# Optimization experiments

Measured on AMD Instinct MI355X. Metric: run time of the kernel, lower is better.

## Reference

```python
import jax, jax.numpy as jnp
import numpy as np

EPS = 1e-6

def rms_norm(x, weight):
    # torch RMSNorm: norm in float32, cast back, then scale
    xf = x.astype(jnp.float32)
    normed = xf * jax.lax.rsqrt(jnp.mean(xf * xf, axis=-1, keepdims=True) + EPS)
    return normed.astype(x.dtype) * weight

def setup_inputs() -> dict:
    B, S, E = 2, 4096, 2048
    H, D, M = 16, 128, 1024  # n_heads, head_dim, memory slots; H*D == E
    key = jax.random.key(0)
    ks = jax.random.split(key, 8)
    std = 0.02
    return {
        "query_input": jax.random.normal(ks[0], (B, S, E), dtype=jnp.float32),
        "W_in": jax.random.normal(ks[1], (H * D, E), dtype=jnp.float32) * std,   # input_proj weight (out,in)
        "W_q": jax.random.normal(ks[2], (D, D), dtype=jnp.float32) * std,
        "W_k": jax.random.normal(ks[3], (D, D), dtype=jnp.float32) * std,
        "W_v": jax.random.normal(ks[4], (D, D), dtype=jnp.float32) * std,
        "stored_patterns": jax.random.normal(ks[5], (H, M, D), dtype=jnp.float32) * std,
        "norm_query_w": jnp.ones((E,), dtype=jnp.float32),
        "norm_retrieved_w": jnp.ones((H * D,), dtype=jnp.float32),
        "beta": jnp.asarray(1.0, dtype=jnp.float32),
    }

def reference(query_input, W_in, W_q, W_k, W_v, stored_patterns,
              norm_query_w, norm_retrieved_w, beta):
    B, S, E = query_input.shape
    H, M, D = stored_patterns.shape
    # RMSNorm + input projection
    normed_q = rms_norm(query_input, norm_query_w)
    proj = normed_q @ W_in.T                       # [B,S,H*D]
    q = proj.reshape(B, S, H, D) @ W_q.T           # [B,S,H,D]
    # memory-bank key/value projections (shared across batch)
    k = stored_patterns @ W_k.T                    # [H,M,D]
    v = stored_patterns @ W_v.T                    # [H,M,D]
    b = jax.nn.sigmoid(beta)                       # clamp_beta=True
    scores = jnp.einsum('bshd,hmd->bhsm', q * b, k)  # [B,H,S,M]
    probs = jax.nn.softmax(scores, axis=-1)
    attn_out = jnp.einsum('bhsm,hmd->bshd', probs, v)  # [B,S,H,D]
    attn_flat = attn_out.reshape(B, S, H * D)
    retrieved = rms_norm(attn_flat, norm_retrieved_w)
    # combine_method == 'add': residual add with original query input
    return retrieved + query_input
```

## Files before the change

### kernel.cpp

```cpp
#include <hip/hip_runtime.h>

typedef unsigned short u16;
typedef unsigned int u32;
typedef __attribute__((ext_vector_type(8))) short bf16x8;
typedef __attribute__((ext_vector_type(4))) float f32x4;
typedef __attribute__((ext_vector_type(16))) float f32x16;

#define B_ 2
#define S_ 4096
#define E_ 2048
#define H_ 16
#define D_ 128
#define M_ 1024
#define N_ROWS (B_*S_)

__device__ __forceinline__ u16 f2bf(float f) {
  unsigned u = __float_as_uint(f);
  u += 0x7FFF + ((u >> 16) & 1);
  return (u16)(u >> 16);
}
__device__ __forceinline__ float bf2f(u16 h) {
  return __uint_as_float(((unsigned)h) << 16);
}
__device__ __forceinline__ void gl_lds16(const u16* g, u16* l) {
  __builtin_amdgcn_global_load_lds(
      (const __attribute__((address_space(1))) u32*)g,
      (__attribute__((address_space(3))) u32*)l, 16, 0, 0);
}

__global__ __launch_bounds__(256) void rmsnorm_to_bf16(
    const float* __restrict__ x, const float* __restrict__ w, u16* __restrict__ out)
{
  int row = blockIdx.x;
  int t = threadIdx.x;
  const float* xr = x + (long)row * E_;
  float4 v0 = *(const float4*)(xr + t*8);
  float4 v1 = *(const float4*)(xr + t*8 + 4);
  float ss = v0.x*v0.x + v0.y*v0.y + v0.z*v0.z + v0.w*v0.w
           + v1.x*v1.x + v1.y*v1.y + v1.z*v1.z + v1.w*v1.w;
  for (int m = 1; m < 64; m <<= 1) ss += __shfl_xor(ss, m);
  __shared__ float red[4];
  if ((t & 63) == 0) red[t >> 6] = ss;
  __syncthreads();
  float tot = red[0] + red[1] + red[2] + red[3];
  float inv = rsqrtf(tot * (1.0f / E_) + 1e-6f);
  float4 w0 = *(const float4*)(w + t*8);
  float4 w1 = *(const float4*)(w + t*8 + 4);
  u16 o[8];
  o[0]=f2bf(v0.x*inv*w0.x); o[1]=f2bf(v0.y*inv*w0.y);
  o[2]=f2bf(v0.z*inv*w0.z); o[3]=f2bf(v0.w*inv*w0.w);
  o[4]=f2bf(v1.x*inv*w1.x); o[5]=f2bf(v1.y*inv*w1.y);
  o[6]=f2bf(v1.z*inv*w1.z); o[7]=f2bf(v1.w*inv*w1.w);
  uint4 pk;
  pk.x = (u32)o[0] | ((u32)o[1] << 16);
  pk.y = (u32)o[2] | ((u32)o[3] << 16);
  pk.z = (u32)o[4] | ((u32)o[5] << 16);
  pk.w = (u32)o[6] | ((u32)o[7] << 16);
  *(uint4*)(out + (long)row*E_ + t*8) = pk;
}

__global__ __launch_bounds__(256) void transpose_to_bf16(
    const float* __restrict__ in, u16* __restrict__ out, int rows, int cols)
{
  __shared__ u16 tile[64*66];
  int c0 = blockIdx.x * 64, r0 = blockIdx.y * 64;
  int t = threadIdx.x;
  for (int i = 0; i < 16; ++i) {
    int idx = i*256 + t;
    int r = idx >> 6, c = idx & 63;
    tile[r*66 + c] = f2bf(in[(long)(r0 + r)*cols + c0 + c]);
  }
  __syncthreads();
  for (int i = 0; i < 16; ++i) {
    int idx = i*256 + t;
    int rr = idx >> 6, cc = idx & 63;
    out[(long)(c0 + rr)*rows + r0 + cc] = tile[cc*66 + rr];
  }
}

__global__ __launch_bounds__(256) void convert_bf16(
    const float* __restrict__ in, u16* __restrict__ out, int n,
    const float* __restrict__ beta)
{
  float sc = 1.0f;
  if (beta) sc = 1.0f / (1.0f + __expf(-beta[0]));
  int i = blockIdx.x*256 + threadIdx.x;
  if (i < n) out[i] = f2bf(in[i] * sc);
}

__global__ __launch_bounds__(256,2) void gemm_bt(
    const u16* __restrict__ A, const u16* __restrict__ Bm, u16* __restrict__ C,
    int K, int lda, int ldb, int ldc, long strA, long strB, long strC)
{
  const int bz = blockIdx.z;
  const u16* Ab = A + bz*strA + (long)blockIdx.y*128*lda;
  const u16* Bb = Bm + bz*strB + (long)blockIdx.x*128*ldb;
  u16* Cb = C + bz*strC + (long)blockIdx.y*128*ldc + blockIdx.x*128;

  __shared__ __align__(16) u16 sA[4*128*8];
  __shared__ __align__(16) u16 sB[4*128*8];

  int tid = threadIdx.x;
  int wave = tid >> 6, lane = tid & 63;
  int wm = wave & 1, wn = wave >> 1;
  int l15 = lane & 15, quad = lane >> 4;

  f32x4 acc[4][4] = {};
  for (int k0 = 0; k0 < K; k0 += 32) {
    __syncthreads();
    gl_lds16(Ab + (long)lane*lda + k0 + wave*8,        &sA[(wave*128 +  0)*8]);
    gl_lds16(Ab + (long)(64+lane)*lda + k0 + wave*8,   &sA[(wave*128 + 64)*8]);
    gl_lds16(Bb + (long)lane*ldb + k0 + wave*8,        &sB[(wave*128 +  0)*8]);
    gl_lds16(Bb + (long)(64+lane)*ldb + k0 + wave*8,   &sB[(wave*128 + 64)*8]);
    __syncthreads();
    bf16x8 af[4], bfg[4];
    for (int i = 0; i < 4; ++i)
      af[i] = *(const bf16x8*)(&sA[(quad*128 + wm*64 + i*16 + l15)*8]);
    for (int j = 0; j < 4; ++j)
      bfg[j] = *(const bf16x8*)(&sB[(quad*128 + wn*64 + j*16 + l15)*8]);
    for (int i = 0; i < 4; ++i)
      for (int j = 0; j < 4; ++j)
        acc[i][j] = __builtin_amdgcn_mfma_f32_16x16x32_bf16(af[i], bfg[j], acc[i][j], 0, 0, 0);
  }
  for (int i = 0; i < 4; ++i)
    for (int j = 0; j < 4; ++j)
      for (int r = 0; r < 4; ++r) {
        int row = wm*64 + i*16 + quad*4 + r;
        int col = wn*64 + j*16 + l15;
        Cb[(long)row*ldc + col] = f2bf(acc[i][j][r]);
      }
}

__global__ __launch_bounds__(256,2) void attention_kernel(
    const u16* __restrict__ q, const u16* __restrict__ k, const u16* __restrict__ vt,
    u16* __restrict__ attn)
{
  int st = blockIdx.x, h = blockIdx.y, b = blockIdx.z;
  int s0 = st * 128;

  __shared__ __align__(16) u16 sQ[16*128*8];
  __shared__ __align__(16) u16 sK[16*64*8];
  __shared__ __align__(16) u16 sV[8*128*8];

  int tid = threadIdx.x;
  int wave = tid >> 6, lane = tid & 63;
  int c31 = lane & 31, hi = lane >> 5;

  const u16* qb  = q  + ((long)(b*S_ + s0))*2048 + h*128;
  const u16* kb  = k  + (long)h*(M_*128);
  const u16* vb  = vt + (long)h*(128*M_);

  for (int i = 0; i < 8; ++i) {
    int c = wave + 4*i;
    int sec = c >> 1, sh = c & 1;
    gl_lds16(qb + (long)(sh*64 + lane)*2048 + sec*8, &sQ[(sec*128 + sh*64)*8]);
  }
  __syncthreads();

  bf16x8 aq[8];
  for (int ks = 0; ks < 8; ++ks)
    aq[ks] = *(const bf16x8*)(&sQ[((ks*2 + hi)*128 + wave*32 + c31)*8]);

  f32x16 O[4];
  for (int dt = 0; dt < 4; ++dt)
    for (int r = 0; r < 16; ++r) O[dt][r] = 0.f;
  float l_run = 0.f;

  for (int mc = 0; mc < 16; ++mc) {
    for (int i = 0; i < 4; ++i) {
      int c = wave + 4*i;
      gl_lds16(kb + (long)(mc*64 + lane)*128 + c*8, &sK[c*64*8]);
      int sec = c >> 1, dh = c & 1;
      gl_lds16(vb + (long)(dh*64 + lane)*M_ + mc*64 + sec*8, &sV[(sec*128 + dh*64)*8]);
    }
    __syncthreads();

    f32x16 sc0, sc1;
    for (int r = 0; r < 16; ++r) { sc0[r] = 0.f; sc1[r] = 0.f; }
    for (int ks = 0; ks < 8; ++ks) {
      bf16x8 ak0 = *(const bf16x8*)(&sK[((ks*2 + hi)*64 +  0 + c31)*8]);
      bf16x8 ak1 = *(const bf16x8*)(&sK[((ks*2 + hi)*64 + 32 + c31)*8]);
      sc0 = __builtin_amdgcn_mfma_f32_32x32x16_bf16(ak0, aq[ks], sc0, 0, 0, 0);
      sc1 = __builtin_amdgcn_mfma_f32_32x32x16_bf16(ak1, aq[ks], sc1, 0, 0, 0);
    }

    bf16x8 pf[4];
    for (int mt = 0; mt < 2; ++mt) {
      f32x16& s = mt ? sc1 : sc0;
      u32 Pk[8];
      float lacc = 0.f;
      for (int p = 0; p < 8; ++p) {
        float e0 = __expf(s[2*p]);
        float e1 = __expf(s[2*p+1]);
        lacc += e0 + e1;
        Pk[p] = (u32)f2bf(e0) | ((u32)f2bf(e1) << 16);
      }
      l_run += lacc;
      u32 X[8];
      for (int p = 0; p < 8; ++p) X[p] = (u32)__shfl_xor((int)Pk[p], 32);
      union { u32 u[4]; bf16x8 v; } f0, f1;
      f0.u[0] = hi ? X[2]  : Pk[0];  f0.u[1] = hi ? X[3]  : Pk[1];
      f0.u[2] = hi ? Pk[2] : X[0];   f0.u[3] = hi ? Pk[3] : X[1];
      f1.u[0] = hi ? X[6]  : Pk[4];  f1.u[1] = hi ? X[7]  : Pk[5];
      f1.u[2] = hi ? Pk[6] : X[4];   f1.u[3] = hi ? Pk[7] : X[5];
      pf[mt*2]   = f0.v;
      pf[mt*2+1] = f1.v;
    }

    for (int ksp = 0; ksp < 4; ++ksp)
      for (int dt = 0; dt < 4; ++dt) {
        bf16x8 bv = *(const bf16x8*)(&sV[((ksp*2 + hi)*128 + dt*32 + c31)*8]);
        O[dt] = __builtin_amdgcn_mfma_f32_32x32x16_bf16(pf[ksp], bv, O[dt], 0, 0, 0);
      }
    __syncthreads();
  }

  l_run += __shfl_xor(l_run, 32);
  float linv = 1.0f / l_run;

  u16* ab = attn + ((long)(b*S_ + s0 + wave*32))*2048 + h*128;
  for (int r = 0; r < 16; ++r) {
    int srow = (r & 3) + 8*(r >> 2) + 4*hi;
    float inv = __shfl(linv, srow);
    long ro = (long)srow * 2048;
    ab[ro +  0 + c31] = f2bf(O[0][r] * inv);
    ab[ro + 32 + c31] = f2bf(O[1][r] * inv);
    ab[ro + 64 + c31] = f2bf(O[2][r] * inv);
    ab[ro + 96 + c31] = f2bf(O[3][r] * inv);
  }
}

__global__ __launch_bounds__(256) void epilogue_kernel(
    const u16* __restrict__ attn, const float* __restrict__ w,
    const float* __restrict__ query, float* __restrict__ out)
{
  int row = blockIdx.x;
  int t = threadIdx.x;
  const u16* ar = attn + (long)row*E_;
  uint4 pk = *(const uint4*)(ar + t*8);
  const u16* ph = (const u16*)&pk;
  float a[8];
  float ss = 0.f;
  for (int i = 0; i < 8; ++i) { a[i] = bf2f(ph[i]); ss += a[i]*a[i]; }
  for (int m = 1; m < 64; m <<= 1) ss += __shfl_xor(ss, m);
  __shared__ float red[4];
  if ((t & 63) == 0) red[t >> 6] = ss;
  __syncthreads();
  float tot = red[0] + red[1] + red[2] + red[3];
  float inv = rsqrtf(tot * (1.0f / E_) + 1e-6f);
  const float* qr = query + (long)row*E_;
  float4 q0 = *(const float4*)(qr + t*8);
  float4 q1 = *(const float4*)(qr + t*8 + 4);
  float4 w0 = *(const float4*)(w + t*8);
  float4 w1 = *(const float4*)(w + t*8 + 4);
  float4 r0, r1;
  r0.x = a[0]*inv*w0.x + q0.x;  r0.y = a[1]*inv*w0.y + q0.y;
  r0.z = a[2]*inv*w0.z + q0.z;  r0.w = a[3]*inv*w0.w + q0.w;
  r1.x = a[4]*inv*w1.x + q1.x;  r1.y = a[5]*inv*w1.y + q1.y;
  r1.z = a[6]*inv*w1.z + q1.z;  r1.w = a[7]*inv*w1.w + q1.w;
  *(float4*)(out + (long)row*E_ + t*8) = r0;
  *(float4*)(out + (long)row*E_ + t*8 + 4) = r1;
}

extern "C" void kernel_launch(void* const* d_in, const int* in_sizes, int n_in,
                              void* d_out, int out_size, void* d_ws, size_t ws_size,
                              hipStream_t stream) {
  const float* query = (const float*)d_in[0];
  const float* W_in  = (const float*)d_in[1];
  const float* W_q   = (const float*)d_in[2];
  const float* W_k   = (const float*)d_in[3];
  const float* W_v   = (const float*)d_in[4];
  const float* sp    = (const float*)d_in[5];
  const float* w_nq  = (const float*)d_in[6];
  const float* w_nr  = (const float*)d_in[7];
  const float* beta  = (const float*)d_in[8];
  float* out = (float*)d_out;

  char* ws = (char*)d_ws;
  u16* normed = (u16*)(ws + 0);
  u16* qbuf   = (u16*)(ws + 33554432);
  u16* Wc     = (u16*)(ws + 67108864);
  u16* WinT   = (u16*)(ws + 75497472);
  u16* spb    = (u16*)(ws + 83886080);
  u16* kbf    = (u16*)(ws + 88080384);
  u16* vtb    = (u16*)(ws + 92274688);
  u16* wqb    = (u16*)(ws + 96468992);
  u16* wkb    = (u16*)(ws + 96501760);
  u16* wvb    = (u16*)(ws + 96534528);
  u16* attn = normed;

  rmsnorm_to_bf16<<<N_ROWS, 256, 0, stream>>>(query, w_nq, normed);
  transpose_to_bf16<<<dim3(32, 32), 256, 0, stream>>>(W_in, WinT, 2048, 2048);
  convert_bf16<<<(H_*M_*D_ + 255)/256, 256, 0, stream>>>(sp, spb, H_*M_*D_, nullptr);
  convert_bf16<<<64, 256, 0, stream>>>(W_q, wqb, D_*D_, beta);
  convert_bf16<<<64, 256, 0, stream>>>(W_k, wkb, D_*D_, nullptr);
  convert_bf16<<<64, 256, 0, stream>>>(W_v, wvb, D_*D_, nullptr);

  gemm_bt<<<dim3(16, 1, 16), 256, 0, stream>>>(wqb, WinT, Wc,
      128, 128, 2048, 2048, 0L, 128L, 262144L);
  gemm_bt<<<dim3(1, 8, 16), 256, 0, stream>>>(spb, wkb, kbf,
      128, 128, 128, 128, 131072L, 0L, 131072L);
  gemm_bt<<<dim3(8, 1, 16), 256, 0, stream>>>(wvb, spb, vtb,
      128, 128, 128, 1024, 0L, 131072L, 131072L);
  gemm_bt<<<dim3(16, 64, 1), 256, 0, stream>>>(normed, Wc, qbuf,
      2048, 2048, 2048, 2048, 0L, 0L, 0L);

  attention_kernel<<<dim3(32, 16, 2), 256, 0, stream>>>(qbuf, kbf, vtb, attn);
  epilogue_kernel<<<N_ROWS, 256, 0, stream>>>(attn, w_nr, query, out);
}
```

Before: 439.1 us.

## Pre-pack GEMM and attention operands into tile-contiguous layouts for coalesced LDS loads

Producers (RMSNorm, the weight/K/V GEMMs, the Q GEMM) now write their outputs in a tile-packed layout matching the LDS fragment order. Consumers (the new gemm_packed and the attention kernel) can then fetch each 16-byte chunk with fully contiguous lane addresses instead of strided row reads. This targets uncoalesced global-to-LDS traffic in the main Q projection and the attention K/V/Q loads. The cost is scattered, strided stores in the producer epilogues and more complex index arithmetic.

```diff
diff --git a/kernel.cpp b/kernel.cpp
--- a/kernel.cpp
+++ b/kernel.cpp
@@ -28,8 +28,8 @@
       (__attribute__((address_space(3))) u32*)l, 16, 0, 0);
 }
 
-__global__ __launch_bounds__(256) void rmsnorm_to_bf16(
-    const float* __restrict__ x, const float* __restrict__ w, u16* __restrict__ out)
+__global__ __launch_bounds__(256) void rmsnorm_to_packed(
+    const float* __restrict__ x, const float* __restrict__ w, u16* __restrict__ outP)
 {
   int row = blockIdx.x;
   int t = threadIdx.x;
@@ -56,7 +56,9 @@
   pk.y = (u32)o[2] | ((u32)o[3] << 16);
   pk.z = (u32)o[4] | ((u32)o[5] << 16);
   pk.w = (u32)o[6] | ((u32)o[7] << 16);
-  *(uint4*)(out + (long)row*E_ + t*8) = pk;
+  int y = row >> 7, lr = row & 127;
+  int kb = t >> 2, sec = t & 3;
+  *(uint4*)(outP + ((long)(y*64 + kb))*4096 + sec*1024 + lr*8) = pk;
 }
 
 __global__ __launch_bounds__(256) void transpose_to_bf16(
@@ -90,12 +92,11 @@
 
 __global__ __launch_bounds__(256,2) void gemm_bt(
     const u16* __restrict__ A, const u16* __restrict__ Bm, u16* __restrict__ C,
-    int K, int lda, int ldb, int ldc, long strA, long strB, long strC)
+    int K, int lda, int ldb, long strA, long strB, int cmode)
 {
   const int bz = blockIdx.z;
   const u16* Ab = A + bz*strA + (long)blockIdx.y*128*lda;
   const u16* Bb = Bm + bz*strB + (long)blockIdx.x*128*ldb;
-  u16* Cb = C + bz*strC + (long)blockIdx.y*128*ldc + blockIdx.x*128;
 
   __shared__ __align__(16) u16 sA[4*128*8];
   __shared__ __align__(16) u16 sB[4*128*8];
@@ -126,13 +127,67 @@
     for (int j = 0; j < 4; ++j)
       for (int r = 0; r < 4; ++r) {
         int row = wm*64 + i*16 + quad*4 + r;
-        int col = wn*64 + j*16 + l15;
-        Cb[(long)row*ldc + col] = f2bf(acc[i][j][r]);
+        int col = blockIdx.x*128 + wn*64 + j*16 + l15;
+        u16 val = f2bf(acc[i][j][r]);
+        long dst;
+        if (cmode == 1) {
+          dst = ((long)(bz*64 + (col>>5)))*4096 + ((col>>3)&3)*1024 + row*8 + (col&7);
+        } else if (cmode == 2) {
+          int m = blockIdx.y*128 + row;
+          dst = ((long)(bz*16 + (m>>6)))*8192 + (col>>3)*512 + (m&63)*8 + (col&7);
+        } else {
+          dst = ((long)(bz*16 + (col>>6)))*8192 + ((col&63)>>3)*1024 + row*8 + (col&7);
+        }
+        C[dst] = val;
       }
 }
 
+__global__ __launch_bounds__(256,2) void gemm_packed(
+    const u16* __restrict__ AP, const u16* __restrict__ BP, u16* __restrict__ qP)
+{
+  const u16* At = AP + (long)blockIdx.y*64*4096;
+  const u16* Bt = BP + (long)blockIdx.x*64*4096;
+
+  __shared__ __align__(16) u16 sA[4*128*8];
+  __shared__ __align__(16) u16 sB[4*128*8];
+
+  int tid = threadIdx.x;
+  int wave = tid >> 6, lane = tid & 63;
+  int wm = wave & 1, wn = wave >> 1;
+  int l15 = lane & 15, quad = lane >> 4;
+
+  f32x4 acc[4][4] = {};
+  for (int ks = 0; ks < 64; ++ks) {
+    __syncthreads();
+    const u16* Ag = At + ks*4096;
+    const u16* Bg = Bt + ks*4096;
+    for (int i = 0; i < 2; ++i) {
+      int cc = wave + i*4;
+      gl_lds16(Ag + cc*512 + lane*8, &sA[cc*512]);
+      gl_lds16(Bg + cc*512 + lane*8, &sB[cc*512]);
+    }
+    __syncthreads();
+    bf16x8 af[4], bfg[4];
+    for (int i = 0; i < 4; ++i)
+      af[i] = *(const bf16x8*)(&sA[(quad*128 + wm*64 + i*16 + l15)*8]);
+    for (int j = 0; j < 4; ++j)
+      bfg[j] = *(const bf16x8*)(&sB[(quad*128 + wn*64 + j*16 + l15)*8]);
+    for (int i = 0; i < 4; ++i)
+      for (int j = 0; j < 4; ++j)
+        acc[i][j] = __builtin_amdgcn_mfma_f32_16x16x32_bf16(af[i], bfg[j], acc[i][j], 0, 0, 0);
+  }
+  u16* qt = qP + ((long)(blockIdx.y*16 + blockIdx.x))*16384;
+  for (int i = 0; i < 4; ++i)
+    for (int j = 0; j < 4; ++j)
+      for (int r = 0; r < 4; ++r) {
+        int row = wm*64 + i*16 + quad*4 + r;
+        int d = wn*64 + j*16 + l15;
+        qt[(d>>3)*1024 + row*8 + (d&7)] = f2bf(acc[i][j][r]);
+      }
+}
+
 __global__ __launch_bounds__(256,2) void attention_kernel(
-    const u16* __restrict__ q, const u16* __restrict__ k, const u16* __restrict__ vt,
+    const u16* __restrict__ qP, const u16* __restrict__ kP, const u16* __restrict__ vP,
     u16* __restrict__ attn)
 {
   int st = blockIdx.x, h = blockIdx.y, b = blockIdx.z;
@@ -146,14 +201,10 @@
   int wave = tid >> 6, lane = tid & 63;
   int c31 = lane & 31, hi = lane >> 5;
 
-  const u16* qb  = q  + ((long)(b*S_ + s0))*2048 + h*128;
-  const u16* kb  = k  + (long)h*(M_*128);
-  const u16* vb  = vt + (long)h*(128*M_);
-
+  const u16* qt = qP + ((long)((b*32 + st)*16 + h))*16384;
   for (int i = 0; i < 8; ++i) {
-    int c = wave + 4*i;
-    int sec = c >> 1, sh = c & 1;
-    gl_lds16(qb + (long)(sh*64 + lane)*2048 + sec*8, &sQ[(sec*128 + sh*64)*8]);
+    int cc = wave + i*4;
+    gl_lds16(qt + cc*512 + lane*8, &sQ[cc*512]);
   }
   __syncthreads();
 
@@ -166,12 +217,16 @@
     for (int r = 0; r < 16; ++r) O[dt][r] = 0.f;
   float l_run = 0.f;
 
+  const u16* kb0 = kP + (long)h*16*8192;
+  const u16* vb0 = vP + (long)h*16*8192;
+
   for (int mc = 0; mc < 16; ++mc) {
+    const u16* kt = kb0 + mc*8192;
+    const u16* vt = vb0 + mc*8192;
     for (int i = 0; i < 4; ++i) {
-      int c = wave + 4*i;
-      gl_lds16(kb + (long)(mc*64 + lane)*128 + c*8, &sK[c*64*8]);
-      int sec = c >> 1, dh = c & 1;
-      gl_lds16(vb + (long)(dh*64 + lane)*M_ + mc*64 + sec*8, &sV[(sec*128 + dh*64)*8]);
+      int cc = wave + i*4;
+      gl_lds16(kt + cc*512 + lane*8, &sK[cc*512]);
+      gl_lds16(vt + cc*512 + lane*8, &sV[cc*512]);
     }
     __syncthreads();
 
@@ -277,34 +332,33 @@
   float* out = (float*)d_out;
 
   char* ws = (char*)d_ws;
-  u16* normed = (u16*)(ws + 0);
-  u16* qbuf   = (u16*)(ws + 33554432);
-  u16* Wc     = (u16*)(ws + 67108864);
-  u16* WinT   = (u16*)(ws + 75497472);
-  u16* spb    = (u16*)(ws + 83886080);
-  u16* kbf    = (u16*)(ws + 88080384);
-  u16* vtb    = (u16*)(ws + 92274688);
-  u16* wqb    = (u16*)(ws + 96468992);
-  u16* wkb    = (u16*)(ws + 96501760);
-  u16* wvb    = (u16*)(ws + 96534528);
-  u16* attn = normed;
-
-  rmsnorm_to_bf16<<<N_ROWS, 256, 0, stream>>>(query, w_nq, normed);
+  u16* normedP = (u16*)(ws + 0);
+  u16* qP      = (u16*)(ws + 33554432);
+  u16* WcP     = (u16*)(ws + 67108864);
+  u16* WinT    = (u16*)(ws + 75497472);
+  u16* spb     = (u16*)(ws + 83886080);
+  u16* kP      = (u16*)(ws + 88080384);
+  u16* vP      = (u16*)(ws + 92274688);
+  u16* wqb     = (u16*)(ws + 96468992);
+  u16* wkb     = (u16*)(ws + 96501760);
+  u16* wvb     = (u16*)(ws + 96534528);
+  u16* attn = normedP;
+
+  rmsnorm_to_packed<<<N_ROWS, 256, 0, stream>>>(query, w_nq, normedP);
   transpose_to_bf16<<<dim3(32, 32), 256, 0, stream>>>(W_in, WinT, 2048, 2048);
   convert_bf16<<<(H_*M_*D_ + 255)/256, 256, 0, stream>>>(sp, spb, H_*M_*D_, nullptr);
   convert_bf16<<<64, 256, 0, stream>>>(W_q, wqb, D_*D_, beta);
   convert_bf16<<<64, 256, 0, stream>>>(W_k, wkb, D_*D_, nullptr);
   convert_bf16<<<64, 256, 0, stream>>>(W_v, wvb, D_*D_, nullptr);
 
-  gemm_bt<<<dim3(16, 1, 16), 256, 0, stream>>>(wqb, WinT, Wc,
-      128, 128, 2048, 2048, 0L, 128L, 262144L);
-  gemm_bt<<<dim3(1, 8, 16), 256, 0, stream>>>(spb, wkb, kbf,
-      128, 128, 128, 128, 131072L, 0L, 131072L);
-  gemm_bt<<<dim3(8, 1, 16), 256, 0, stream>>>(wvb, spb, vtb,
-      128, 128, 128, 1024, 0L, 131072L, 131072L);
-  gemm_bt<<<dim3(16, 64, 1), 256, 0, stream>>>(normed, Wc, qbuf,
-      2048, 2048, 2048, 2048, 0L, 0L, 0L);
-
-  attention_kernel<<<dim3(32, 16, 2), 256, 0, stream>>>(qbuf, kbf, vtb, attn);
+  gemm_bt<<<dim3(16, 1, 16), 256, 0, stream>>>(wqb, WinT, WcP,
+      128, 128, 2048, 0L, 128L, 1);
+  gemm_bt<<<dim3(1, 8, 16), 256, 0, stream>>>(spb, wkb, kP,
+      128, 128, 128, 131072L, 0L, 2);
+  gemm_bt<<<dim3(8, 1, 16), 256, 0, stream>>>(wvb, spb, vP,
+      128, 128, 128, 0L, 131072L, 3);
+  gemm_packed<<<dim3(16, 64), 256, 0, stream>>>(normedP, WcP, qP);
+
+  attention_kernel<<<dim3(32, 16, 2), 256, 0, stream>>>(qP, kP, vP, attn);
   epilogue_kernel<<<N_ROWS, 256, 0, stream>>>(attn, w_nr, query, out);
 }
```

Result: faster. 386.4 us (-12.0%).
